# Performance work log

Measured on AMD Instinct MI355X. Metric: run time of the kernel, lower is better.

The kernel has to match this reference:

```python
import jax, jax.numpy as jnp
import numpy as np

BATCH = 4096
DIM = 512
NOISE_POWER = 1.0


def setup_inputs() -> dict:
    key = jax.random.key(0)
    k1, k2 = jax.random.split(key)
    info = jax.random.normal(k1, (BATCH, DIM), dtype=jnp.float32)
    codewords = jax.random.normal(k2, (BATCH, DIM), dtype=jnp.float32)
    sigma = (NOISE_POWER * jnp.eye(DIM, dtype=jnp.float32))
    return {"info": info, "codewords": codewords, "sigma": sigma}


def _gmm_entropy_upper(mu, sigma):
    """Kolchinsky-style upper bound on Gaussian-mixture entropy.

    Faithful to tensor_entropy_gauss_mix_upper: pairwise Mahalanobis
    quadratic form exponent[i, j] = -0.5 * (mu_i - mu_j)^T Sig^-1 (mu_i - mu_j),
    computed via the Gram-matrix expansion instead of materializing the
    [B*B, dim] repeat/tile intermediates.
    """
    B, dim = mu.shape
    sig_inv = jnp.linalg.inv(sigma)
    A = mu @ sig_inv                      # [B, dim]
    q = jnp.sum(A * mu, axis=1)           # [B] diagonal quadratic terms
    G = A @ mu.T                          # [B, B]  mu_i Sig^-1 mu_j^T
    # expo[i, j] = -0.5*(q_i + q_j - G[i,j] - G[j,i])
    expo = -0.5 * (q[:, None] + q[None, :] - G - G.T)
    lse = jax.nn.logsumexp(expo, axis=1)  # [B], over mixture components j
    weight = 1.0 / B
    factor_log = -(dim / 2.0) * jnp.log(2.0 * jnp.pi * sigma[0, 0])
    log_inner = jnp.log(weight) + factor_log + lse
    entropy = dim / 2.0 - jnp.sum(weight * log_inner)
    return entropy


def reference(info, codewords, sigma):
    # Original call: info, codewords = inputs; info_codewords = codewords
    # (info is unpacked but unused). h_z and h_zm both use codewords.
    h_z = _gmm_entropy_upper(codewords, sigma)
    h_zm = _gmm_entropy_upper(codewords, sigma)
    return jnp.stack([h_z, h_zm])
```

## Files before the change

### kernel.cpp

```cpp
#include <hip/hip_runtime.h>
#include <math.h>

#define NB 4096
#define ND 512
#define TILE 128
#define NCP 8

typedef float floatx4 __attribute__((ext_vector_type(4)));
typedef long longx2 __attribute__((ext_vector_type(2)));
typedef unsigned int uint;

__device__ inline unsigned char enc_e4m3(float x) {
    unsigned bits = __float_as_uint(x);
    unsigned sign = (bits >> 31) << 7;
    float ax = fabsf(x);
    if (ax < 0.015625f) {
        int m = (int)(ax * 512.0f + 0.5f);
        return (unsigned char)(sign | m);
    }
    int e = (int)((bits >> 23) & 0xFF) - 127;
    unsigned r = ((bits & 0x7FFFFF) + 0x80000) >> 20;
    if (r == 8) { r = 0; e += 1; }
    if (e > 8) { e = 8; r = 7; }
    return (unsigned char)(sign | ((unsigned)(e + 7) << 3) | r);
}

__device__ inline float dec_e4m3(unsigned char b) {
    int e = (b >> 3) & 0xF;
    int m = b & 7;
    float mag = e ? ldexpf(1.0f + (float)m * 0.125f, e - 7)
                  : ldexpf((float)m * 0.125f, -6);
    return (b & 0x80) ? -mag : mag;
}


__global__ __launch_bounds__(256) void prep_kernel(const float* __restrict__ mu,
                                                   unsigned char* __restrict__ muf8,
                                                   float* __restrict__ hq,
                                                   float* __restrict__ sumexp) {
    const int t = threadIdx.x;
    const int wave = t >> 6, lane = t & 63;
    const int row = blockIdx.x * 4 + wave;
    const float4* src = (const float4*)(mu + (size_t)row * ND) + lane * 2;
    const float4 v0 = src[0], v1 = src[1];
    unsigned char b[8];
    b[0] = enc_e4m3(v0.x); b[1] = enc_e4m3(v0.y);
    b[2] = enc_e4m3(v0.z); b[3] = enc_e4m3(v0.w);
    b[4] = enc_e4m3(v1.x); b[5] = enc_e4m3(v1.y);
    b[6] = enc_e4m3(v1.z); b[7] = enc_e4m3(v1.w);
    uint lo = (uint)b[0] | ((uint)b[1] << 8) | ((uint)b[2] << 16) | ((uint)b[3] << 24);
    uint hi = (uint)b[4] | ((uint)b[5] << 8) | ((uint)b[6] << 16) | ((uint)b[7] << 24);
    const size_t unit = ((size_t)(row >> 4) * 8 + (lane >> 3)) * 64
                      + (size_t)(lane & 3) * 16 + (row & 15);
    uint2 pk; pk.x = lo; pk.y = hi;
    *(uint2*)(muf8 + unit * 16 + ((lane >> 2) & 1) * 8) = pk;
    float sq = 0.0f;
    #pragma unroll
    for (int e = 0; e < 8; e++) { float f = dec_e4m3(b[e]); sq += f * f; }
    #pragma unroll
    for (int off = 32; off > 0; off >>= 1) sq += __shfl_down(sq, off, 64);
    if (lane == 0) {
        hq[row] = 0.5f * sq;
        sumexp[row] = 0.0f;
    }
}

__global__ __launch_bounds__(256) void gram_lse_kernel(const unsigned char* __restrict__ muf8,
                                                       const float* __restrict__ hq,
                                                       const float* __restrict__ sigma,
                                                       float* __restrict__ sumexp) {
    const int t = threadIdx.x;
    const int wave = t >> 6;
    const int lane = t & 63;
    const int r16 = lane & 15;
    const int quad = lane >> 4;

    const int bswz = blockIdx.x;
    const int x = bswz & 7, s = bswz >> 3;
    const int by = (x >> 2) * 16 + (s & 15);
    const int bx = (x & 3) * 8 + (s >> 4);

    const int row0 = by * TILE + (wave >> 1) * 64;
    const int col0 = bx * TILE + (wave & 1) * 64;

    const longx2* base = (const longx2*)muf8;
    const longx2* pA[4];
    const longx2* pB[4];
    #pragma unroll
    for (int i = 0; i < 4; i++)
        pA[i] = base + ((size_t)(row0 / 16 + i) * 8) * 64 + lane;
    #pragma unroll
    for (int j = 0; j < 4; j++)
        pB[j] = base + ((size_t)(col0 / 16 + j) * 8) * 64 + lane;

    floatx4 acc[4][4];
    #pragma unroll
    for (int i = 0; i < 4; i++)
        #pragma unroll
        for (int j = 0; j < 4; j++) {
            floatx4 z = {0.f, 0.f, 0.f, 0.f};
            acc[i][j] = z;
        }

    longx2 fa[2][4], fb[2][4];
    #pragma unroll
    for (int i = 0; i < 4; i++) fa[0][i] = pA[i][0];
    #pragma unroll
    for (int j = 0; j < 4; j++) fb[0][j] = pB[j][0];

    #pragma unroll
    for (int cp = 0; cp < NCP; cp++) {
        const int cur = cp & 1, nxt = cur ^ 1;
        if (cp < NCP - 1) {
            #pragma unroll
            for (int i = 0; i < 4; i++) fa[nxt][i] = pA[i][(cp + 1) * 64];
            #pragma unroll
            for (int j = 0; j < 4; j++) fb[nxt][j] = pB[j][(cp + 1) * 64];
        }
        #pragma unroll
        for (int i = 0; i < 4; i++)
            #pragma unroll
            for (int j = 0; j < 4; j++)
                acc[i][j] = __builtin_amdgcn_mfma_f32_16x16x32_fp8_fp8(fa[cur][i][0], fb[cur][j][0], acc[i][j], 0, 0, 0);
        #pragma unroll
        for (int i = 0; i < 4; i++)
            #pragma unroll
            for (int j = 0; j < 4; j++)
                acc[i][j] = __builtin_amdgcn_mfma_f32_16x16x32_fp8_fp8(fa[cur][i][1], fb[cur][j][1], acc[i][j], 0, 0, 0);
    }

    const float inv_s = 1.0f / sigma[0];
    float hqc[4];
    #pragma unroll
    for (int j = 0; j < 4; j++) hqc[j] = hq[col0 + j * 16 + r16];

    #pragma unroll
    for (int i = 0; i < 4; i++) {
        #pragma unroll
        for (int r = 0; r < 4; r++) {
            const int row = row0 + i * 16 + quad * 4 + r;
            const float hr = hq[row];
            float rs = 0.0f;
            #pragma unroll
            for (int j = 0; j < 4; j++)
                rs += __expf((acc[i][j][r] - hr - hqc[j]) * inv_s);
            rs += __shfl_xor(rs, 1, 64);
            rs += __shfl_xor(rs, 2, 64);
            rs += __shfl_xor(rs, 4, 64);
            rs += __shfl_xor(rs, 8, 64);
            if (r16 == 0) atomicAdd(&sumexp[row], rs);
        }
    }
}

__global__ __launch_bounds__(1024) void finalize_kernel(const float* __restrict__ sumexp,
                                                        const float* __restrict__ sigma,
                                                        float* __restrict__ out) {
    const int t = threadIdx.x;
    float local = 0.0f;
    for (int i = t; i < NB; i += 1024) local += logf(sumexp[i]);
    #pragma unroll
    for (int off = 32; off > 0; off >>= 1) local += __shfl_down(local, off, 64);
    __shared__ float red[16];
    if ((t & 63) == 0) red[t >> 6] = local;
    __syncthreads();
    if (t == 0) {
        double tot = 0.0;
        #pragma unroll
        for (int i = 0; i < 16; i++) tot += (double)red[i];
        const double s = (double)sigma[0];
        const double ent = (double)(ND / 2)
                         + log((double)NB)
                         + (double)(ND / 2) * log(2.0 * M_PI * s)
                         - tot / (double)NB;
        out[0] = (float)ent;
        out[1] = (float)ent;
    }
}

extern "C" void kernel_launch(void* const* d_in, const int* in_sizes, int n_in,
                              void* d_out, int out_size, void* d_ws, size_t ws_size,
                              hipStream_t stream) {
    (void)in_sizes; (void)n_in; (void)out_size; (void)ws_size;
    const float* codewords = (const float*)d_in[1];
    const float* sigma     = (const float*)d_in[2];
    float* out = (float*)d_out;

    char* ws = (char*)d_ws;
    unsigned char* muf8 = (unsigned char*)ws;
    float* hq     = (float*)(ws + (size_t)NB * ND);
    float* sumexp = hq + NB;

    prep_kernel<<<NB / 4, 256, 0, stream>>>(codewords, muf8, hq, sumexp);
    gram_lse_kernel<<<1024, 256, 0, stream>>>(muf8, hq, sigma, sumexp);
    finalize_kernel<<<1, 1024, 0, stream>>>(sumexp, sigma, out);
}
```

Before: 93.68 us.

## Stage fp8 Gram tiles in LDS via async global-to-LDS loads

The Gram kernel no longer has each wave load its A/B fragments straight from global memory into registers. The whole block now cooperatively copies the 128-row A and B panels for each K-chunk into a 32KB shared buffer using global_load_lds. Waves then read their fragments from LDS, so the two waves that share a panel no longer both fetch it from global memory. The cost is two barriers per chunk with no double buffering, which removes the previous register-level prefetch overlap between loads and MFMA.

```diff
diff --git a/kernel.cpp b/kernel.cpp
--- a/kernel.cpp
+++ b/kernel.cpp
@@ -4,11 +4,16 @@
 #define NB 4096
 #define ND 512
 #define TILE 128
-#define NCP 8
+#define NE 4
 
 typedef float floatx4 __attribute__((ext_vector_type(4)));
 typedef long longx2 __attribute__((ext_vector_type(2)));
 typedef unsigned int uint;
+
+__device__ inline void async_load16(const void* g, void* l) {
+    __builtin_amdgcn_global_load_lds((const __attribute__((address_space(1))) void*)g,
+                                     (__attribute__((address_space(3))) void*)l, 16, 0, 0);
+}
 
 __device__ inline unsigned char enc_e4m3(float x) {
     unsigned bits = __float_as_uint(x);
@@ -69,6 +74,8 @@
                                                        const float* __restrict__ hq,
                                                        const float* __restrict__ sigma,
                                                        float* __restrict__ sumexp) {
+    __shared__ alignas(16) unsigned char smem[32768];
+
     const int t = threadIdx.x;
     const int wave = t >> 6;
     const int lane = t & 63;
@@ -80,18 +87,10 @@
     const int by = (x >> 2) * 16 + (s & 15);
     const int bx = (x & 3) * 8 + (s >> 4);
 
+    const int apan = by * (TILE / 16);
+    const int bpan = bx * (TILE / 16);
     const int row0 = by * TILE + (wave >> 1) * 64;
     const int col0 = bx * TILE + (wave & 1) * 64;
-
-    const longx2* base = (const longx2*)muf8;
-    const longx2* pA[4];
-    const longx2* pB[4];
-    #pragma unroll
-    for (int i = 0; i < 4; i++)
-        pA[i] = base + ((size_t)(row0 / 16 + i) * 8) * 64 + lane;
-    #pragma unroll
-    for (int j = 0; j < 4; j++)
-        pB[j] = base + ((size_t)(col0 / 16 + j) * 8) * 64 + lane;
 
     floatx4 acc[4][4];
     #pragma unroll
@@ -102,31 +101,41 @@
             acc[i][j] = z;
         }
 
-    longx2 fa[2][4], fb[2][4];
-    #pragma unroll
-    for (int i = 0; i < 4; i++) fa[0][i] = pA[i][0];
-    #pragma unroll
-    for (int j = 0; j < 4; j++) fb[0][j] = pB[j][0];
-
-    #pragma unroll
-    for (int cp = 0; cp < NCP; cp++) {
-        const int cur = cp & 1, nxt = cur ^ 1;
-        if (cp < NCP - 1) {
-            #pragma unroll
-            for (int i = 0; i < 4; i++) fa[nxt][i] = pA[i][(cp + 1) * 64];
-            #pragma unroll
-            for (int j = 0; j < 4; j++) fb[nxt][j] = pB[j][(cp + 1) * 64];
-        }
-        #pragma unroll
-        for (int i = 0; i < 4; i++)
+    for (int e = 0; e < NE; e++) {
+        __syncthreads();
+        #pragma unroll
+        for (int sw = 0; sw < 8; sw++) {
+            const int idx = sw * 256 + t;
+            const int sel = idx >> 10;
+            const int k = idx & 1023;
+            const int pi = k >> 7;
+            const int rest = k & 127;
+            const int pan = (sel ? bpan : apan) + pi;
+            const size_t gu = ((size_t)pan * 8 + 2 * e + (rest >> 6)) * 64 + (rest & 63);
+            async_load16(muf8 + gu * 16, smem + (size_t)idx * 16);
+        }
+        __syncthreads();
+
+        #pragma unroll
+        for (int c = 0; c < 2; c++) {
+            longx2 a[4], b[4];
+            #pragma unroll
+            for (int i = 0; i < 4; i++)
+                a[i] = *(const longx2*)(smem + ((((wave >> 1) * 4 + i) * 2 + c) * 64 + lane) * 16);
             #pragma unroll
             for (int j = 0; j < 4; j++)
-                acc[i][j] = __builtin_amdgcn_mfma_f32_16x16x32_fp8_fp8(fa[cur][i][0], fb[cur][j][0], acc[i][j], 0, 0, 0);
-        #pragma unroll
-        for (int i = 0; i < 4; i++)
-            #pragma unroll
-            for (int j = 0; j < 4; j++)
-                acc[i][j] = __builtin_amdgcn_mfma_f32_16x16x32_fp8_fp8(fa[cur][i][1], fb[cur][j][1], acc[i][j], 0, 0, 0);
+                b[j] = *(const longx2*)(smem + 16384 + ((((wave & 1) * 4 + j) * 2 + c) * 64 + lane) * 16);
+            #pragma unroll
+            for (int i = 0; i < 4; i++)
+                #pragma unroll
+                for (int j = 0; j < 4; j++)
+                    acc[i][j] = __builtin_amdgcn_mfma_f32_16x16x32_fp8_fp8(a[i][0], b[j][0], acc[i][j], 0, 0, 0);
+            #pragma unroll
+            for (int i = 0; i < 4; i++)
+                #pragma unroll
+                for (int j = 0; j < 4; j++)
+                    acc[i][j] = __builtin_amdgcn_mfma_f32_16x16x32_fp8_fp8(a[i][1], b[j][1], acc[i][j], 0, 0, 0);
+        }
     }
 
     const float inv_s = 1.0f / sigma[0];
```

Result: slower. 100.6 us (+7.4%).

## Fuse finalize into gram kernel via last-block counter and deepen prefetch

Applied to the files above, without the earlier changes.

Drops the separate finalize launch. The gram kernel now counts finished blocks with an atomic counter (reset in prep), and the last block to finish computes the log-sum and writes the entropy, using release/acquire fences around the counter. The fragment loads are also restructured to a two-stage-ahead prefetch, issued after the MFMAs, so loads overlap with more compute. This saves a launch and its tail latency, at the cost of a serial reduction in one 256-thread block and extra fence overhead in every block.

```diff
diff --git a/kernel.cpp b/kernel.cpp
--- a/kernel.cpp
+++ b/kernel.cpp
@@ -5,6 +5,7 @@
 #define ND 512
 #define TILE 128
 #define NCP 8
+#define NBLK 1024
 
 typedef float floatx4 __attribute__((ext_vector_type(4)));
 typedef long longx2 __attribute__((ext_vector_type(2)));
@@ -37,7 +38,8 @@
 __global__ __launch_bounds__(256) void prep_kernel(const float* __restrict__ mu,
                                                    unsigned char* __restrict__ muf8,
                                                    float* __restrict__ hq,
-                                                   float* __restrict__ sumexp) {
+                                                   float* __restrict__ sumexp,
+                                                   unsigned* __restrict__ counter) {
     const int t = threadIdx.x;
     const int wave = t >> 6, lane = t & 63;
     const int row = blockIdx.x * 4 + wave;
@@ -63,12 +65,15 @@
         hq[row] = 0.5f * sq;
         sumexp[row] = 0.0f;
     }
+    if (blockIdx.x == 0 && t == 0) *counter = 0u;
 }
 
 __global__ __launch_bounds__(256) void gram_lse_kernel(const unsigned char* __restrict__ muf8,
                                                        const float* __restrict__ hq,
                                                        const float* __restrict__ sigma,
-                                                       float* __restrict__ sumexp) {
+                                                       float* __restrict__ sumexp,
+                                                       unsigned* __restrict__ counter,
+                                                       float* __restrict__ out) {
     const int t = threadIdx.x;
     const int wave = t >> 6;
     const int lane = t & 63;
@@ -107,16 +112,14 @@
     for (int i = 0; i < 4; i++) fa[0][i] = pA[i][0];
     #pragma unroll
     for (int j = 0; j < 4; j++) fb[0][j] = pB[j][0];
+    #pragma unroll
+    for (int i = 0; i < 4; i++) fa[1][i] = pA[i][64];
+    #pragma unroll
+    for (int j = 0; j < 4; j++) fb[1][j] = pB[j][64];
 
     #pragma unroll
     for (int cp = 0; cp < NCP; cp++) {
-        const int cur = cp & 1, nxt = cur ^ 1;
-        if (cp < NCP - 1) {
-            #pragma unroll
-            for (int i = 0; i < 4; i++) fa[nxt][i] = pA[i][(cp + 1) * 64];
-            #pragma unroll
-            for (int j = 0; j < 4; j++) fb[nxt][j] = pB[j][(cp + 1) * 64];
-        }
+        const int cur = cp & 1;
         #pragma unroll
         for (int i = 0; i < 4; i++)
             #pragma unroll
@@ -127,6 +130,12 @@
             #pragma unroll
             for (int j = 0; j < 4; j++)
                 acc[i][j] = __builtin_amdgcn_mfma_f32_16x16x32_fp8_fp8(fa[cur][i][1], fb[cur][j][1], acc[i][j], 0, 0, 0);
+        if (cp + 2 < NCP) {
+            #pragma unroll
+            for (int i = 0; i < 4; i++) fa[cur][i] = pA[i][(cp + 2) * 64];
+            #pragma unroll
+            for (int j = 0; j < 4; j++) fb[cur][j] = pB[j][(cp + 2) * 64];
+        }
     }
 
     const float inv_s = 1.0f / sigma[0];
@@ -151,30 +160,32 @@
             if (r16 == 0) atomicAdd(&sumexp[row], rs);
         }
     }
-}
-
-__global__ __launch_bounds__(1024) void finalize_kernel(const float* __restrict__ sumexp,
-                                                        const float* __restrict__ sigma,
-                                                        float* __restrict__ out) {
-    const int t = threadIdx.x;
-    float local = 0.0f;
-    for (int i = t; i < NB; i += 1024) local += logf(sumexp[i]);
-    #pragma unroll
-    for (int off = 32; off > 0; off >>= 1) local += __shfl_down(local, off, 64);
-    __shared__ float red[16];
-    if ((t & 63) == 0) red[t >> 6] = local;
+
+    __builtin_amdgcn_fence(__ATOMIC_RELEASE, "agent");
     __syncthreads();
-    if (t == 0) {
-        double tot = 0.0;
-        #pragma unroll
-        for (int i = 0; i < 16; i++) tot += (double)red[i];
-        const double s = (double)sigma[0];
-        const double ent = (double)(ND / 2)
-                         + log((double)NB)
-                         + (double)(ND / 2) * log(2.0 * M_PI * s)
-                         - tot / (double)NB;
-        out[0] = (float)ent;
-        out[1] = (float)ent;
+    __shared__ unsigned done;
+    if (t == 0)
+        done = __hip_atomic_fetch_add(counter, 1u, __ATOMIC_RELAXED, __HIP_MEMORY_SCOPE_AGENT);
+    __syncthreads();
+    if (done == NBLK - 1) {
+        __builtin_amdgcn_fence(__ATOMIC_ACQUIRE, "agent");
+        float local = 0.0f;
+        for (int i = t; i < NB; i += 256) local += logf(sumexp[i]);
+        #pragma unroll
+        for (int off = 32; off > 0; off >>= 1) local += __shfl_down(local, off, 64);
+        __shared__ float fred[4];
+        if ((t & 63) == 0) fred[t >> 6] = local;
+        __syncthreads();
+        if (t == 0) {
+            const double tot = (double)fred[0] + fred[1] + fred[2] + fred[3];
+            const double sg = (double)sigma[0];
+            const double ent = (double)(ND / 2)
+                             + log((double)NB)
+                             + (double)(ND / 2) * log(2.0 * M_PI * sg)
+                             - tot / (double)NB;
+            out[0] = (float)ent;
+            out[1] = (float)ent;
+        }
     }
 }
 
@@ -190,8 +201,8 @@
     unsigned char* muf8 = (unsigned char*)ws;
     float* hq     = (float*)(ws + (size_t)NB * ND);
     float* sumexp = hq + NB;
-
-    prep_kernel<<<NB / 4, 256, 0, stream>>>(codewords, muf8, hq, sumexp);
-    gram_lse_kernel<<<1024, 256, 0, stream>>>(muf8, hq, sigma, sumexp);
-    finalize_kernel<<<1, 1024, 0, stream>>>(sumexp, sigma, out);
-}
+    unsigned* counter = (unsigned*)(sumexp + NB);
+
+    prep_kernel<<<NB / 4, 256, 0, stream>>>(codewords, muf8, hq, sumexp, counter);
+    gram_lse_kernel<<<NBLK, 256, 0, stream>>>(muf8, hq, sigma, sumexp, counter, out);
+}
```

New measurement: 126.4 us. 1.35x slower.
